# Optimization experiments

Hardware: AMD Instinct MI355X
Metric: run time of the kernel (lower is better)

Reference implementation:

```python
import jax, jax.numpy as jnp
import numpy as np

N = 100000          # nodes
E = 1600000         # edges (before self-loops)
F_IN = 512          # num_node_features
H1, C1 = 8, 8       # layer-1 heads, per-head channels
NUM_CLASSES = 40
NEG_SLOPE = 0.2     # PyG GATConv default


def setup_inputs() -> dict:
    key = jax.random.key(0)
    ks = jax.random.split(key, 10)
    x = jax.random.normal(ks[0], (N, F_IN), jnp.float32)
    edge_index = jax.random.randint(ks[1], (2, E), 0, N, dtype=jnp.int64)
    # Glorot-ish scaled params (matches PyG init scale qualitatively)
    W1 = jax.random.normal(ks[2], (F_IN, H1 * C1), jnp.float32) / np.sqrt(F_IN)
    a_src1 = jax.random.normal(ks[3], (H1, C1), jnp.float32) / np.sqrt(C1)
    a_dst1 = jax.random.normal(ks[4], (H1, C1), jnp.float32) / np.sqrt(C1)
    b1 = jnp.zeros((H1 * C1,), jnp.float32)
    W2 = jax.random.normal(ks[5], (H1 * C1, NUM_CLASSES), jnp.float32) / np.sqrt(H1 * C1)
    a_src2 = jax.random.normal(ks[6], (1, NUM_CLASSES), jnp.float32) / np.sqrt(NUM_CLASSES)
    a_dst2 = jax.random.normal(ks[7], (1, NUM_CLASSES), jnp.float32) / np.sqrt(NUM_CLASSES)
    b2 = jnp.zeros((NUM_CLASSES,), jnp.float32)
    return {"x": x, "edge_index": edge_index, "W1": W1, "a_src1": a_src1,
            "a_dst1": a_dst1, "b1": b1, "W2": W2, "a_src2": a_src2,
            "a_dst2": a_dst2, "b2": b2}


def gat_layer(x, src, dst, W, a_s, a_d, b, concat):
    """PyG GATConv (eval mode: dropout=0). src -> dst messages, softmax over dst."""
    heads, ch = a_s.shape
    n = x.shape[0]
    h = (x @ W).reshape(n, heads, ch)                      # [N,H,C]
    alpha_s = jnp.einsum('nhc,hc->nh', h, a_s)             # [N,H]
    alpha_d = jnp.einsum('nhc,hc->nh', h, a_d)
    e = jax.nn.leaky_relu(alpha_s[src] + alpha_d[dst], NEG_SLOPE)   # [E,H]
    # segment softmax over incoming edges of each dst node
    m = jax.ops.segment_max(e, dst, num_segments=n)        # [N,H]
    p = jnp.exp(e - m[dst])
    s = jax.ops.segment_sum(p, dst, num_segments=n)
    alpha = p / (s[dst] + 1e-16)                           # [E,H]
    out = jax.ops.segment_sum(h[src] * alpha[..., None], dst, num_segments=n)  # [N,H,C]
    out = out.reshape(n, heads * ch) if concat else out.mean(axis=1)
    return out + b


def reference(x, edge_index, W1, a_src1, a_dst1, b1, W2, a_src2, a_dst2, b2):
    n = x.shape[0]
    loops = jnp.arange(n, dtype=edge_index.dtype)
    src = jnp.concatenate([edge_index[0], loops])          # add self-loops (PyG default)
    dst = jnp.concatenate([edge_index[1], loops])
    h = gat_layer(x, src, dst, W1, a_src1, a_dst1, b1, concat=True)
    h = jax.nn.elu(h)
    out = gat_layer(h, src, dst, W2, a_src2, a_dst2, b2, concat=False)
    return jax.nn.log_softmax(out, axis=1)
```

## Files before the change

### kernel.cpp

```cpp
#include <hip/hip_runtime.h>
#include <hip/hip_bf16.h>
#include <hip/hip_fp16.h>

#define F_IN 512
#define HC1 64
#define NH1 8
#define NC 40
#define NEG_SLOPE 0.2f
#define SCAN_CHUNK 2048
#define RADIX_EPB 4096
#define MAXNB 512
#define BCAP 8192

typedef short bf16x8 __attribute__((ext_vector_type(8)));
typedef float f32x4 __attribute__((ext_vector_type(4)));

static __device__ __forceinline__ unsigned short f2b(float f) {
    __hip_bfloat16 h = __float2bfloat16(f);
    return *(unsigned short*)&h;
}
static __device__ __forceinline__ float b2f(unsigned short u) {
    union { unsigned int i; float f; } v;
    v.i = ((unsigned int)u) << 16;
    return v.f;
}
static __device__ __forceinline__ unsigned short f2h(float f) {
    __half h = __float2half(f);
    return *(unsigned short*)&h;
}

__device__ __forceinline__ float lrelu(float e) { return e > 0.f ? e : NEG_SLOPE * e; }

__global__ void prep(const float* __restrict__ W1, const float* __restrict__ W2,
                     const float* __restrict__ a_s2, const float* __restrict__ a_d2,
                     const int* __restrict__ ei,
                     unsigned short* __restrict__ wst, float* __restrict__ ws2,
                     float* __restrict__ wd2, int* __restrict__ flag) {
    if (blockIdx.x == 16) {
        __shared__ int found;
        if (threadIdx.x == 0) found = 0;
        __syncthreads();
        for (int i = threadIdx.x; i < 4096; i += 256) {
            if (ei[2 * i + 1] != 0) atomicOr(&found, 1);
        }
        __syncthreads();
        if (threadIdx.x == 0) *flag = (found == 0) ? 1 : 0;
        return;
    }
    int t = blockIdx.x * 256 + threadIdx.x;
    {
        int p  = t & 7;
        int n  = (t >> 3) & 63;
        int kb = t >> 9;
        int l  = p ^ (n & 7);
        int k0 = kb * 64 + l * 8;
        unsigned short v[8];
#pragma unroll
        for (int j = 0; j < 8; j++) v[j] = f2b(W1[(size_t)(k0 + j) * HC1 + n]);
        *(uint4*)(wst + ((size_t)(kb * 64 + n) * 64 + p * 8)) = *(uint4*)v;
    }
    if (blockIdx.x == 0 && threadIdx.x < HC1) {
        int c = threadIdx.x;
        float s = 0.f, d = 0.f;
#pragma unroll
        for (int j = 0; j < NC; j++) {
            float w = W2[c * NC + j];
            s += w * a_s2[j];
            d += w * a_d2[j];
        }
        ws2[c] = s;
        wd2[c] = d;
    }
}

__global__ __launch_bounds__(256) void scatter1(const int* __restrict__ ei, const int* __restrict__ flag,
                                                int* __restrict__ deg, int* __restrict__ bcnt,
                                                int* __restrict__ bpk, int E, int NB) {
    __shared__ int cnt[MAXNB];
    __shared__ int gb[MAXNB];
    int tid = threadIdx.x;
    for (int i = tid; i < NB; i += 256) cnt[i] = 0;
    __syncthreads();
    int f = *flag;
    int base = blockIdx.x * RADIX_EPB;
    int pk[16], bk[16], rv[16];
#pragma unroll
    for (int i = 0; i < 16; i++) {
        int e = base + i * 256 + tid;
        if (e < E) {
            int s, d;
            if (f) { s = ei[2 * e]; d = ei[2 * (E + e)]; }
            else   { s = ei[e];     d = ei[E + e]; }
            pk[i] = (s << 8) | (d & 255);
            bk[i] = d >> 8;
            rv[i] = atomicAdd(&cnt[bk[i]], 1);
            atomicAdd(&deg[d], 1);
        }
    }
    __syncthreads();
    for (int i = tid; i < NB; i += 256) {
        int c = cnt[i];
        gb[i] = c ? atomicAdd(&bcnt[i], c) : 0;
    }
    __syncthreads();
#pragma unroll
    for (int i = 0; i < 16; i++) {
        int e = base + i * 256 + tid;
        if (e < E) {
            int pos = gb[bk[i]] + rv[i];
            if (pos < BCAP)
                bpk[(size_t)bk[i] * BCAP + pos] = pk[i];
        }
    }
}

__global__ __launch_bounds__(256) void scan1(const int* __restrict__ deg, int* __restrict__ rowptr,
                                             int* __restrict__ bsums, int n) {
    __shared__ int sbuf[256];
    int tid = threadIdx.x;
    int base = blockIdx.x * SCAN_CHUNK + tid * 8;
    int v[8];
#pragma unroll
    for (int j = 0; j < 8; j++) { int idx = base + j; v[j] = (idx < n) ? deg[idx] : 0; }
    int tsum = 0;
#pragma unroll
    for (int j = 0; j < 8; j++) tsum += v[j];
    sbuf[tid] = tsum;
    __syncthreads();
    for (int off = 1; off < 256; off <<= 1) {
        int t = (tid >= off) ? sbuf[tid - off] : 0;
        __syncthreads();
        sbuf[tid] += t;
        __syncthreads();
    }
    int run = sbuf[tid] - tsum;
#pragma unroll
    for (int j = 0; j < 8; j++) {
        run += v[j];
        int idx = base + j;
        if (idx < n) rowptr[1 + idx] = run;
    }
    if (tid == 255) bsums[blockIdx.x] = sbuf[255];
}

__global__ __launch_bounds__(256) void scan23(int* __restrict__ rowptr,
                                              const int* __restrict__ bsums, int n, int nb) {
    __shared__ int soff[64];
    int tid = threadIdx.x;
    if (tid < 64) {
        int lane = tid;
        int v = (lane < nb) ? bsums[lane] : 0;
        int orig = v;
        for (int off = 1; off < 64; off <<= 1) {
            int t = __shfl_up(v, (unsigned)off, 64);
            if (lane >= off) v += t;
        }
        soff[lane] = v - orig;
    }
    __syncthreads();
    int i = blockIdx.x * 256 + tid;
    if (i < n) {
        rowptr[1 + i] += soff[i >> 11];
        if (i == 0) rowptr[0] = 0;
    }
}

__global__ __launch_bounds__(256) void scatter2(const int* __restrict__ bpk,
                                                const int* __restrict__ bcnt,
                                                const int* __restrict__ rowptr,
                                                int* __restrict__ col, int Nn) {
    __shared__ int cur[256];
    int b = blockIdx.x;
    int node0 = b << 8;
    int tid = threadIdx.x;
    int nlast = min(node0 + 256, Nn);
    if (node0 + tid < nlast) cur[tid] = rowptr[node0 + tid];
    __syncthreads();
    int cnt = min(bcnt[b], BCAP);
    const int* bp = bpk + (size_t)b * BCAP;
    for (int j = tid; j < cnt; j += 256) {
        int pk = bp[j];
        int pos = atomicAdd(&cur[pk & 255], 1);
        col[pos] = (int)((unsigned)pk >> 8);
    }
}

__global__ __launch_bounds__(256) void gemm1(const float* __restrict__ x,
                                             const unsigned short* __restrict__ wst,
                                             const float* __restrict__ a_s, const float* __restrict__ a_d,
                                             unsigned short* __restrict__ h1, float* __restrict__ as1,
                                             float* __restrict__ ad1, int Nn) {
    __shared__ __align__(16) unsigned short smem[8192];
    unsigned short* xs = smem;
    unsigned short* ws = smem + 4096;
    int tid = threadIdx.x;
    int m0 = blockIdx.x * 64;
    int w = tid >> 6, lane = tid & 63;
    int quad = lane >> 4, mr = lane & 15;
    f32x4 acc[4];
#pragma unroll
    for (int i = 0; i < 4; i++) acc[i] = (f32x4){0.f, 0.f, 0.f, 0.f};

    int srow = tid >> 2;
    int sseg = tid & 3;
    bool rok = (m0 + srow) < Nn;
    const float* xrow = x + (size_t)(m0 + srow) * F_IN + sseg * 16;
    int swzw = (srow & 7) << 4;
    int swzr = (mr & 7) << 4;

    for (int kb = 0; kb < 8; kb++) {
        float4 xv0, xv1, xv2, xv3;
        if (rok) {
            const float4* xp = (const float4*)(xrow + kb * 64);
            xv0 = xp[0]; xv1 = xp[1]; xv2 = xp[2]; xv3 = xp[3];
        } else {
            xv0 = xv1 = xv2 = xv3 = make_float4(0.f, 0.f, 0.f, 0.f);
        }
        const uint4* wp = (const uint4*)(wst + (size_t)kb * 4096);
        uint4 wv0 = wp[tid];
        uint4 wv1 = wp[tid + 256];
        __syncthreads();
        {
            unsigned short bx[16];
            bx[0]  = f2b(xv0.x); bx[1]  = f2b(xv0.y); bx[2]  = f2b(xv0.z); bx[3]  = f2b(xv0.w);
            bx[4]  = f2b(xv1.x); bx[5]  = f2b(xv1.y); bx[6]  = f2b(xv1.z); bx[7]  = f2b(xv1.w);
            bx[8]  = f2b(xv2.x); bx[9]  = f2b(xv2.y); bx[10] = f2b(xv2.z); bx[11] = f2b(xv2.w);
            bx[12] = f2b(xv3.x); bx[13] = f2b(xv3.y); bx[14] = f2b(xv3.z); bx[15] = f2b(xv3.w);
            unsigned short* xr = xs + srow * 64;
            *(uint4*)(xr + ((((sseg * 32)      ) ^ swzw) >> 1)) = *(uint4*)&bx[0];
            *(uint4*)(xr + ((((sseg * 32) + 16 ) ^ swzw) >> 1)) = *(uint4*)&bx[8];
            ((uint4*)ws)[tid]       = wv0;
            ((uint4*)ws)[tid + 256] = wv1;
        }
        __syncthreads();
#pragma unroll
        for (int ks = 0; ks < 2; ks++) {
            int kc = ks * 64 + quad * 16;
            int co = (kc ^ swzr) >> 1;
            bf16x8 a = *(const bf16x8*)(xs + (w * 16 + mr) * 64 + co);
#pragma unroll
            for (int nb = 0; nb < 4; nb++) {
                bf16x8 b = *(const bf16x8*)(ws + (nb * 16 + mr) * 64 + co);
                acc[nb] = __builtin_amdgcn_mfma_f32_16x16x32_bf16(a, b, acc[nb], 0, 0, 0);
            }
        }
    }
    __syncthreads();
    unsigned short (*hs)[72] = (unsigned short(*)[72])smem;
#pragma unroll
    for (int nb = 0; nb < 4; nb++)
#pragma unroll
        for (int r = 0; r < 4; r++)
            hs[w * 16 + quad * 4 + r][nb * 16 + mr] = f2b(acc[nb][r]);
    __syncthreads();
    {
        if (rok) {
            uint4 v0 = *(const uint4*)&hs[srow][sseg * 16];
            uint4 v1 = *(const uint4*)&hs[srow][sseg * 16 + 8];
            uint4* dst = (uint4*)(h1 + (size_t)(m0 + srow) * HC1 + sseg * 16);
            dst[0] = v0;
            dst[1] = v1;
        }
    }
    for (int i = tid; i < 512; i += 256) {
        int row = i >> 3, hh = i & 7;
        if (m0 + row < Nn) {
            float s = 0.f, d = 0.f;
#pragma unroll
            for (int c = 0; c < 8; c++) {
                float v = b2f(hs[row][hh * 8 + c]);
                s += v * a_s[hh * 8 + c];
                d += v * a_d[hh * 8 + c];
            }
            as1[(size_t)(m0 + row) * NH1 + hh] = s;
            ad1[(size_t)(m0 + row) * NH1 + hh] = d;
        }
    }
}

__global__ __launch_bounds__(256) void agg1(const unsigned short* __restrict__ h1,
                                            const float* __restrict__ as1,
                                            const float* __restrict__ ad1, const int* __restrict__ rowptr,
                                            const int* __restrict__ col, const float* __restrict__ b1,
                                            const float* __restrict__ ws2, const float* __restrict__ wd2,
                                            unsigned short* __restrict__ h2b, float* __restrict__ as2,
                                            float* __restrict__ ad2, int Nn) {
    __shared__ float pbuf[4][NH1 * 68];
    int w = threadIdx.x >> 6;
    int wave = (blockIdx.x * 256 + threadIdx.x) >> 6;
    int lane = threadIdx.x & 63;
    if (wave >= Nn) return;
    int d = wave;
    int jb = rowptr[d], je = rowptr[d + 1];
    int half = lane >> 5;
    int cl = lane & 31;
    int head = cl >> 2;
    const float4* as4 = (const float4*)as1;
    const float4* ad4 = (const float4*)ad1;

    float4 dd0 = ad4[d * 2], dd1 = ad4[d * 2 + 1];
    float adh[8] = {dd0.x, dd0.y, dd0.z, dd0.w, dd1.x, dd1.y, dd1.z, dd1.w};
    float4 sd0 = as4[d * 2], sd1 = as4[d * 2 + 1];
    float svh[8] = {sd0.x, sd0.y, sd0.z, sd0.w, sd1.x, sd1.y, sd1.z, sd1.w};
    float e0[8];
#pragma unroll
    for (int h = 0; h < NH1; h++) e0[h] = lrelu(svh[h] + adh[h]);

    float acc0, acc1, ss;
    {
        unsigned gv = *(const unsigned*)(h1 + (size_t)d * HC1 + 2 * cl);
        union { unsigned i; float f; } lo, hi;
        lo.i = gv << 16; hi.i = gv & 0xffff0000u;
        if (half == 0) { acc0 = lo.f; acc1 = hi.f; ss = 1.f; }
        else           { acc0 = 0.f;  acc1 = 0.f;  ss = 0.f; }
    }
    float* pb = pbuf[w];

    for (int c0 = jb; c0 < je; c0 += 64) {
        int nc = min(64, je - c0);
        int srcv = d;
        if (lane < nc) {
            unsigned u = (unsigned)col[c0 + lane];
            srcv = (u < (unsigned)Nn) ? (int)u : d;
            float4 a0 = as4[srcv * 2], a1 = as4[srcv * 2 + 1];
            float ev[8] = {a0.x, a0.y, a0.z, a0.w, a1.x, a1.y, a1.z, a1.w};
#pragma unroll
            for (int h = 0; h < NH1; h++)
                pb[h * 68 + lane] = __expf(lrelu(ev[h] + adh[h]) - e0[h]);
        } else {
#pragma unroll
            for (int h = 0; h < NH1; h++) pb[h * 68 + lane] = 0.f;
        }
        int ncp = (nc + 15) & ~15;
        for (int jj = 0; jj < ncp; jj += 16) {
            int sarr[8];
            float parr[8];
            unsigned gvv[8];
#pragma unroll
            for (int u4 = 0; u4 < 8; u4++) {
                int idx = jj + 2 * u4 + half;
                sarr[u4] = __shfl(srcv, idx, 64);
                parr[u4] = pb[head * 68 + idx];
            }
#pragma unroll
            for (int u4 = 0; u4 < 8; u4++)
                gvv[u4] = *(const unsigned*)(h1 + (size_t)sarr[u4] * HC1 + 2 * cl);
#pragma unroll
            for (int u4 = 0; u4 < 8; u4++) {
                union { unsigned i; float f; } lo, hi;
                lo.i = gvv[u4] << 16; hi.i = gvv[u4] & 0xffff0000u;
                acc0 += parr[u4] * lo.f;
                acc1 += parr[u4] * hi.f;
                ss += parr[u4];
            }
        }
    }
    acc0 += __shfl_xor(acc0, 32, 64);
    acc1 += __shfl_xor(acc1, 32, 64);
    ss   += __shfl_xor(ss, 32, 64);
    float inv = 1.f / (ss + 1e-16f);
    float o0 = acc0 * inv + b1[2 * cl];
    float o1 = acc1 * inv + b1[2 * cl + 1];
    o0 = o0 > 0.f ? o0 : __expf(o0) - 1.0f;
    o1 = o1 > 0.f ? o1 : __expf(o1) - 1.0f;
    if (half == 0) {
        unsigned pk = (unsigned)f2h(o0) | ((unsigned)f2h(o1) << 16);
        *(unsigned*)(h2b + (size_t)d * HC1 + 2 * cl) = pk;
    }
    float va = o0 * ws2[2 * cl] + o1 * ws2[2 * cl + 1];
    float vd = o0 * wd2[2 * cl] + o1 * wd2[2 * cl + 1];
#pragma unroll
    for (int off = 16; off; off >>= 1) {
        va += __shfl_xor(va, off, 64);
        vd += __shfl_xor(vd, off, 64);
    }
    if (lane == 0) { as2[d] = va; ad2[d] = vd; }
}

__global__ __launch_bounds__(256) void agg2(const unsigned short* __restrict__ h2b,
                                            const float* __restrict__ as2,
                                            const float* __restrict__ ad2, const int* __restrict__ rowptr,
                                            const int* __restrict__ col, const float* __restrict__ W2,
                                            const float* __restrict__ b2,
                                            float* __restrict__ out, int Nn) {
    __shared__ float pbuf[4][64];
    __shared__ float smv[4][64];
    __shared__ float W2s[HC1 * NC];
    int tid = threadIdx.x;
    for (int i = tid; i < HC1 * NC; i += 256) W2s[i] = W2[i];
    __syncthreads();
    int w = tid >> 6;
    int wave = (blockIdx.x * 256 + tid) >> 6;
    int lane = tid & 63;
    if (wave >= Nn) return;
    int d = wave;
    int jb = rowptr[d], je = rowptr[d + 1];
    int half = lane >> 5;
    int cl = lane & 31;
    float adv = ad2[d];
    float e0 = lrelu(as2[d] + adv);
    float acc0, acc1, ss;
    {
        unsigned gv = *(const unsigned*)(h2b + (size_t)d * HC1 + 2 * cl);
        union { unsigned u; __half2 h; } cv; cv.u = gv;
        float2 ff = __half22float2(cv.h);
        if (half == 0) { acc0 = ff.x; acc1 = ff.y; ss = 1.f; }
        else           { acc0 = 0.f;  acc1 = 0.f;  ss = 0.f; }
    }
    float* pb = pbuf[w];

    for (int c0 = jb; c0 < je; c0 += 64) {
        int nc = min(64, je - c0);
        int srcv = d;
        if (lane < nc) {
            unsigned u = (unsigned)col[c0 + lane];
            srcv = (u < (unsigned)Nn) ? (int)u : d;
            pb[lane] = __expf(lrelu(as2[srcv] + adv) - e0);
        } else {
            pb[lane] = 0.f;
        }
        int ncp = (nc + 15) & ~15;
        for (int jj = 0; jj < ncp; jj += 16) {
            int sarr[8];
            float parr[8];
            unsigned gvv[8];
#pragma unroll
            for (int u4 = 0; u4 < 8; u4++) {
                int idx = jj + 2 * u4 + half;
                sarr[u4] = __shfl(srcv, idx, 64);
                parr[u4] = pb[idx];
            }
#pragma unroll
            for (int u4 = 0; u4 < 8; u4++)
                gvv[u4] = *(const unsigned*)(h2b + (size_t)sarr[u4] * HC1 + 2 * cl);
#pragma unroll
            for (int u4 = 0; u4 < 8; u4++) {
                union { unsigned u; __half2 h; } cv; cv.u = gvv[u4];
                float2 ff = __half22float2(cv.h);
                acc0 += parr[u4] * ff.x;
                acc1 += parr[u4] * ff.y;
                ss += parr[u4];
            }
        }
    }
    acc0 += __shfl_xor(acc0, 32, 64);
    acc1 += __shfl_xor(acc1, 32, 64);
    ss   += __shfl_xor(ss, 32, 64);
    float inv = 1.f / (ss + 1e-16f);
    if (half == 0) {
        smv[w][2 * cl]     = acc0 * inv;
        smv[w][2 * cl + 1] = acc1 * inv;
    }
    float o = 0.f;
    if (lane < NC) {
        o = b2[lane];
        const float* sv = smv[w];
#pragma unroll
        for (int c = 0; c < HC1; c++) o += sv[c] * W2s[c * NC + lane];
    }
    float vm = (lane < NC) ? o : -1e30f;
#pragma unroll
    for (int off = 32; off; off >>= 1) vm = fmaxf(vm, __shfl_xor(vm, off, 64));
    float ex = (lane < NC) ? __expf(o - vm) : 0.f;
#pragma unroll
    for (int off = 32; off; off >>= 1) ex += __shfl_xor(ex, off, 64);
    float lsm = o - vm - __logf(ex);
    if (lane < NC) out[(size_t)d * NC + lane] = lsm;
}

extern "C" void kernel_launch(void* const* d_in, const int* in_sizes, int n_in,
                              void* d_out, int out_size, void* d_ws, size_t ws_size,
                              hipStream_t stream) {
    const float* x      = (const float*)d_in[0];
    const int*   ei     = (const int*)d_in[1];
    const float* W1     = (const float*)d_in[2];
    const float* a_src1 = (const float*)d_in[3];
    const float* a_dst1 = (const float*)d_in[4];
    const float* b1     = (const float*)d_in[5];
    const float* W2     = (const float*)d_in[6];
    const float* a_src2 = (const float*)d_in[7];
    const float* a_dst2 = (const float*)d_in[8];
    const float* b2     = (const float*)d_in[9];
    float* out = (float*)d_out;

    const int N = in_sizes[0] / F_IN;
    const int E = in_sizes[1] / 2;
    const int NB = (N + 255) >> 8;

    char* p = (char*)d_ws;
    auto alloc = [&](size_t bytes) -> void* {
        void* r = (void*)p;
        p += (bytes + 255) & ~(size_t)255;
        return r;
    };
    int* deg    = (int*)alloc((size_t)N * 4);
    int* bcnt   = (int*)alloc((size_t)MAXNB * 4);
    int* rowptr = (int*)alloc(((size_t)N + 1) * 4);
    int* bsums  = (int*)alloc(64 * 4);
    int* flag   = (int*)alloc(256);
    int* bpk    = (int*)alloc((size_t)NB * BCAP * 4);
    int* col    = (int*)alloc((size_t)E * 4);
    unsigned short* h1  = (unsigned short*)alloc((size_t)N * HC1 * 2);
    float* as1  = (float*)alloc((size_t)N * NH1 * 4);
    float* ad1  = (float*)alloc((size_t)N * NH1 * 4);
    unsigned short* h2b = (unsigned short*)alloc((size_t)N * HC1 * 2);
    float* as2  = (float*)alloc((size_t)N * 4);
    float* ad2  = (float*)alloc((size_t)N * 4);
    unsigned short* wst = (unsigned short*)alloc(8 * 64 * 64 * 2);
    float* ws2  = (float*)alloc(HC1 * 4);
    float* wd2  = (float*)alloc(HC1 * 4);

    size_t zlen = (size_t)((char*)(bcnt + MAXNB) - (char*)deg);
    hipMemsetAsync(deg, 0, zlen, stream);
    prep<<<17, 256, 0, stream>>>(W1, W2, a_src2, a_dst2, ei, wst, ws2, wd2, flag);
    scatter1<<<(E + RADIX_EPB - 1) / RADIX_EPB, 256, 0, stream>>>(ei, flag, deg, bcnt, bpk, E, NB);
    int nb = (N + SCAN_CHUNK - 1) / SCAN_CHUNK;
    scan1<<<nb, 256, 0, stream>>>(deg, rowptr, bsums, N);
    scan23<<<(N + 255) / 256, 256, 0, stream>>>(rowptr, bsums, N, nb);
    scatter2<<<NB, 256, 0, stream>>>(bpk, bcnt, rowptr, col, N);

    gemm1<<<(N + 63) / 64, 256, 0, stream>>>(x, wst, a_src1, a_dst1, h1, as1, ad1, N);
    agg1<<<(N + 3) / 4, 256, 0, stream>>>(h1, as1, ad1, rowptr, col, b1, ws2, wd2, h2b, as2, ad2, N);

    agg2<<<(N + 3) / 4, 256, 0, stream>>>(h2b, as2, ad2, rowptr, col, W2, b2, out, N);
}
```

Baseline: 581.8 us.

## Split feature channels into four slices and aggregate each slice in its own pass

The hidden features and attention logits move to a slice-major layout: four slices of 16 channels, each 32 bytes per node. Aggregation for both layers runs as four per-slice kernel launches, so each pass gathers from a smaller working set that fits in cache better. Layer 2 writes unnormalised partial sums to a float buffer, and a separate fin kernel applies the normalisation, the W2 projection and log-softmax. In exchange, the edge list and attention exponentials are re-read and recomputed in every pass, there are more launches, and layer-2 logits are accumulated across passes with atomics.

```diff
diff --git a/kernel.cpp b/kernel.cpp
--- a/kernel.cpp
+++ b/kernel.cpp
@@ -27,6 +27,10 @@
 static __device__ __forceinline__ unsigned short f2h(float f) {
     __half h = __float2half(f);
     return *(unsigned short*)&h;
+}
+static __device__ __forceinline__ float h2f(unsigned short u) {
+    __half h = *(__half*)&u;
+    return __half2float(h);
 }
 
 __device__ __forceinline__ float lrelu(float e) { return e > 0.f ? e : NEG_SLOPE * e; }
@@ -188,8 +192,8 @@
 __global__ __launch_bounds__(256) void gemm1(const float* __restrict__ x,
                                              const unsigned short* __restrict__ wst,
                                              const float* __restrict__ a_s, const float* __restrict__ a_d,
-                                             unsigned short* __restrict__ h1, float* __restrict__ as1,
-                                             float* __restrict__ ad1, int Nn) {
+                                             unsigned short* __restrict__ h1s, float* __restrict__ as1s,
+                                             float* __restrict__ ad1s, int Nn) {
     __shared__ __align__(16) unsigned short smem[8192];
     unsigned short* xs = smem;
     unsigned short* ws = smem + 4096;
@@ -257,7 +261,7 @@
         if (rok) {
             uint4 v0 = *(const uint4*)&hs[srow][sseg * 16];
             uint4 v1 = *(const uint4*)&hs[srow][sseg * 16 + 8];
-            uint4* dst = (uint4*)(h1 + (size_t)(m0 + srow) * HC1 + sseg * 16);
+            uint4* dst = (uint4*)(h1s + ((size_t)sseg * Nn + (m0 + srow)) * 16);
             dst[0] = v0;
             dst[1] = v1;
         }
@@ -272,120 +276,140 @@
                 s += v * a_s[hh * 8 + c];
                 d += v * a_d[hh * 8 + c];
             }
-            as1[(size_t)(m0 + row) * NH1 + hh] = s;
-            ad1[(size_t)(m0 + row) * NH1 + hh] = d;
-        }
-    }
-}
-
-__global__ __launch_bounds__(256) void agg1(const unsigned short* __restrict__ h1,
-                                            const float* __restrict__ as1,
-                                            const float* __restrict__ ad1, const int* __restrict__ rowptr,
-                                            const int* __restrict__ col, const float* __restrict__ b1,
-                                            const float* __restrict__ ws2, const float* __restrict__ wd2,
-                                            unsigned short* __restrict__ h2b, float* __restrict__ as2,
-                                            float* __restrict__ ad2, int Nn) {
-    __shared__ float pbuf[4][NH1 * 68];
-    int w = threadIdx.x >> 6;
+            size_t idx = ((size_t)(hh >> 1) * Nn + (m0 + row)) * 2 + (hh & 1);
+            as1s[idx] = s;
+            ad1s[idx] = d;
+        }
+    }
+}
+
+__global__ __launch_bounds__(256) void agg1p(const unsigned short* __restrict__ h1s,
+                                             const float* __restrict__ as1s,
+                                             const float* __restrict__ ad1s,
+                                             const int* __restrict__ rowptr, const int* __restrict__ col,
+                                             const float* __restrict__ b1,
+                                             const float* __restrict__ ws2, const float* __restrict__ wd2,
+                                             unsigned short* __restrict__ h2s, float* __restrict__ as2,
+                                             float* __restrict__ ad2, int Nn, int k) {
     int wave = (blockIdx.x * 256 + threadIdx.x) >> 6;
     int lane = threadIdx.x & 63;
     if (wave >= Nn) return;
     int d = wave;
+    int g = lane >> 3, cl = lane & 7;
+    int hl = cl >> 2;
+    const unsigned short* hsl = h1s + (size_t)k * Nn * 16;
+    const float* asl = as1s + (size_t)k * Nn * 2;
+    const float* adl = ad1s + (size_t)k * Nn * 2;
+    float adv = adl[(size_t)d * 2 + hl];
+    float e0 = lrelu(asl[(size_t)d * 2 + hl] + adv);
     int jb = rowptr[d], je = rowptr[d + 1];
-    int half = lane >> 5;
-    int cl = lane & 31;
-    int head = cl >> 2;
-    const float4* as4 = (const float4*)as1;
-    const float4* ad4 = (const float4*)ad1;
-
-    float4 dd0 = ad4[d * 2], dd1 = ad4[d * 2 + 1];
-    float adh[8] = {dd0.x, dd0.y, dd0.z, dd0.w, dd1.x, dd1.y, dd1.z, dd1.w};
-    float4 sd0 = as4[d * 2], sd1 = as4[d * 2 + 1];
-    float svh[8] = {sd0.x, sd0.y, sd0.z, sd0.w, sd1.x, sd1.y, sd1.z, sd1.w};
-    float e0[8];
-#pragma unroll
-    for (int h = 0; h < NH1; h++) e0[h] = lrelu(svh[h] + adh[h]);
-
-    float acc0, acc1, ss;
-    {
-        unsigned gv = *(const unsigned*)(h1 + (size_t)d * HC1 + 2 * cl);
-        union { unsigned i; float f; } lo, hi;
-        lo.i = gv << 16; hi.i = gv & 0xffff0000u;
-        if (half == 0) { acc0 = lo.f; acc1 = hi.f; ss = 1.f; }
-        else           { acc0 = 0.f;  acc1 = 0.f;  ss = 0.f; }
-    }
-    float* pb = pbuf[w];
-
-    for (int c0 = jb; c0 < je; c0 += 64) {
-        int nc = min(64, je - c0);
-        int srcv = d;
-        if (lane < nc) {
-            unsigned u = (unsigned)col[c0 + lane];
-            srcv = (u < (unsigned)Nn) ? (int)u : d;
-            float4 a0 = as4[srcv * 2], a1 = as4[srcv * 2 + 1];
-            float ev[8] = {a0.x, a0.y, a0.z, a0.w, a1.x, a1.y, a1.z, a1.w};
-#pragma unroll
-            for (int h = 0; h < NH1; h++)
-                pb[h * 68 + lane] = __expf(lrelu(ev[h] + adh[h]) - e0[h]);
-        } else {
-#pragma unroll
-            for (int h = 0; h < NH1; h++) pb[h * 68 + lane] = 0.f;
-        }
-        int ncp = (nc + 15) & ~15;
-        for (int jj = 0; jj < ncp; jj += 16) {
-            int sarr[8];
-            float parr[8];
-            unsigned gvv[8];
-#pragma unroll
-            for (int u4 = 0; u4 < 8; u4++) {
-                int idx = jj + 2 * u4 + half;
-                sarr[u4] = __shfl(srcv, idx, 64);
-                parr[u4] = pb[head * 68 + idx];
-            }
-#pragma unroll
-            for (int u4 = 0; u4 < 8; u4++)
-                gvv[u4] = *(const unsigned*)(h1 + (size_t)sarr[u4] * HC1 + 2 * cl);
-#pragma unroll
-            for (int u4 = 0; u4 < 8; u4++) {
-                union { unsigned i; float f; } lo, hi;
-                lo.i = gvv[u4] << 16; hi.i = gvv[u4] & 0xffff0000u;
-                acc0 += parr[u4] * lo.f;
-                acc1 += parr[u4] * hi.f;
-                ss += parr[u4];
-            }
-        }
-    }
-    acc0 += __shfl_xor(acc0, 32, 64);
-    acc1 += __shfl_xor(acc1, 32, 64);
-    ss   += __shfl_xor(ss, 32, 64);
-    float inv = 1.f / (ss + 1e-16f);
-    float o0 = acc0 * inv + b1[2 * cl];
-    float o1 = acc1 * inv + b1[2 * cl + 1];
-    o0 = o0 > 0.f ? o0 : __expf(o0) - 1.0f;
-    o1 = o1 > 0.f ? o1 : __expf(o1) - 1.0f;
-    if (half == 0) {
+    float acc0 = 0.f, acc1 = 0.f, ss = 0.f;
+    if (g == 0) {
+        unsigned gv = *(const unsigned*)(hsl + (size_t)d * 16 + 2 * cl);
+        acc0 = b2f((unsigned short)(gv & 0xffff));
+        acc1 = b2f((unsigned short)(gv >> 16));
+        ss = 1.f;
+    }
+    for (int c = jb; c < je; c += 16) {
+        int eA = c + g, eB = c + 8 + g;
+        bool vA = eA < je, vB = eB < je;
+        int sA = d, sB = d;
+        if (vA) { unsigned u = (unsigned)col[eA]; sA = (u < (unsigned)Nn) ? (int)u : d; }
+        if (vB) { unsigned u = (unsigned)col[eB]; sB = (u < (unsigned)Nn) ? (int)u : d; }
+        float aA = asl[(size_t)sA * 2 + hl];
+        float aB = asl[(size_t)sB * 2 + hl];
+        unsigned gA = *(const unsigned*)(hsl + (size_t)sA * 16 + 2 * cl);
+        unsigned gB = *(const unsigned*)(hsl + (size_t)sB * 16 + 2 * cl);
+        float pA = vA ? __expf(lrelu(aA + adv) - e0) : 0.f;
+        float pB = vB ? __expf(lrelu(aB + adv) - e0) : 0.f;
+        acc0 += pA * b2f((unsigned short)(gA & 0xffff)) + pB * b2f((unsigned short)(gB & 0xffff));
+        acc1 += pA * b2f((unsigned short)(gA >> 16))   + pB * b2f((unsigned short)(gB >> 16));
+        ss += pA + pB;
+    }
+#pragma unroll
+    for (int off = 8; off <= 32; off <<= 1) {
+        acc0 += __shfl_xor(acc0, off, 64);
+        acc1 += __shfl_xor(acc1, off, 64);
+        ss   += __shfl_xor(ss, off, 64);
+    }
+    if (g == 0) {
+        float inv = 1.f / (ss + 1e-16f);
+        float o0 = acc0 * inv + b1[k * 16 + 2 * cl];
+        float o1 = acc1 * inv + b1[k * 16 + 2 * cl + 1];
+        o0 = o0 > 0.f ? o0 : __expf(o0) - 1.0f;
+        o1 = o1 > 0.f ? o1 : __expf(o1) - 1.0f;
         unsigned pk = (unsigned)f2h(o0) | ((unsigned)f2h(o1) << 16);
-        *(unsigned*)(h2b + (size_t)d * HC1 + 2 * cl) = pk;
-    }
-    float va = o0 * ws2[2 * cl] + o1 * ws2[2 * cl + 1];
-    float vd = o0 * wd2[2 * cl] + o1 * wd2[2 * cl + 1];
-#pragma unroll
-    for (int off = 16; off; off >>= 1) {
-        va += __shfl_xor(va, off, 64);
-        vd += __shfl_xor(vd, off, 64);
-    }
-    if (lane == 0) { as2[d] = va; ad2[d] = vd; }
-}
-
-__global__ __launch_bounds__(256) void agg2(const unsigned short* __restrict__ h2b,
-                                            const float* __restrict__ as2,
-                                            const float* __restrict__ ad2, const int* __restrict__ rowptr,
-                                            const int* __restrict__ col, const float* __restrict__ W2,
-                                            const float* __restrict__ b2,
-                                            float* __restrict__ out, int Nn) {
-    __shared__ float pbuf[4][64];
-    __shared__ float smv[4][64];
+        *(unsigned*)(h2s + ((size_t)k * Nn + d) * 16 + 2 * cl) = pk;
+        float va = o0 * ws2[k * 16 + 2 * cl] + o1 * ws2[k * 16 + 2 * cl + 1];
+        float vd = o0 * wd2[k * 16 + 2 * cl] + o1 * wd2[k * 16 + 2 * cl + 1];
+#pragma unroll
+        for (int off = 1; off <= 4; off <<= 1) {
+            va += __shfl_xor(va, off, 64);
+            vd += __shfl_xor(vd, off, 64);
+        }
+        if (lane == 0) {
+            if (k == 0) { as2[d] = va; ad2[d] = vd; }
+            else        { atomicAdd(&as2[d], va); atomicAdd(&ad2[d], vd); }
+        }
+    }
+}
+
+__global__ __launch_bounds__(256) void agg2p(const unsigned short* __restrict__ h2s,
+                                             const float* __restrict__ as2,
+                                             const float* __restrict__ ad2,
+                                             const int* __restrict__ rowptr, const int* __restrict__ col,
+                                             float* __restrict__ hbar, float* __restrict__ ssum2,
+                                             int Nn, int k) {
+    int wave = (blockIdx.x * 256 + threadIdx.x) >> 6;
+    int lane = threadIdx.x & 63;
+    if (wave >= Nn) return;
+    int d = wave;
+    int g = lane >> 3, cl = lane & 7;
+    const unsigned short* hsl = h2s + (size_t)k * Nn * 16;
+    float adv = ad2[d];
+    float e0 = lrelu(as2[d] + adv);
+    int jb = rowptr[d], je = rowptr[d + 1];
+    float acc0 = 0.f, acc1 = 0.f, ss = 0.f;
+    if (g == 0) {
+        unsigned gv = *(const unsigned*)(hsl + (size_t)d * 16 + 2 * cl);
+        acc0 = h2f((unsigned short)(gv & 0xffff));
+        acc1 = h2f((unsigned short)(gv >> 16));
+        ss = 1.f;
+    }
+    for (int c = jb; c < je; c += 16) {
+        int eA = c + g, eB = c + 8 + g;
+        bool vA = eA < je, vB = eB < je;
+        int sA = d, sB = d;
+        if (vA) { unsigned u = (unsigned)col[eA]; sA = (u < (unsigned)Nn) ? (int)u : d; }
+        if (vB) { unsigned u = (unsigned)col[eB]; sB = (u < (unsigned)Nn) ? (int)u : d; }
+        float aA = as2[sA];
+        float aB = as2[sB];
+        unsigned gA = *(const unsigned*)(hsl + (size_t)sA * 16 + 2 * cl);
+        unsigned gB = *(const unsigned*)(hsl + (size_t)sB * 16 + 2 * cl);
+        float pA = vA ? __expf(lrelu(aA + adv) - e0) : 0.f;
+        float pB = vB ? __expf(lrelu(aB + adv) - e0) : 0.f;
+        acc0 += pA * h2f((unsigned short)(gA & 0xffff)) + pB * h2f((unsigned short)(gB & 0xffff));
+        acc1 += pA * h2f((unsigned short)(gA >> 16))   + pB * h2f((unsigned short)(gB >> 16));
+        ss += pA + pB;
+    }
+#pragma unroll
+    for (int off = 8; off <= 32; off <<= 1) {
+        acc0 += __shfl_xor(acc0, off, 64);
+        acc1 += __shfl_xor(acc1, off, 64);
+        ss   += __shfl_xor(ss, off, 64);
+    }
+    if (g == 0) {
+        *(float2*)(hbar + ((size_t)k * Nn + d) * 16 + 2 * cl) = make_float2(acc0, acc1);
+        if (k == 0 && cl == 0) ssum2[d] = ss;
+    }
+}
+
+__global__ __launch_bounds__(256) void fin(const float* __restrict__ hbar,
+                                           const float* __restrict__ ssum2,
+                                           const float* __restrict__ W2, const float* __restrict__ b2,
+                                           float* __restrict__ out, int Nn) {
     __shared__ float W2s[HC1 * NC];
+    __shared__ float hv[4][HC1];
     int tid = threadIdx.x;
     for (int i = tid; i < HC1 * NC; i += 256) W2s[i] = W2[i];
     __syncthreads();
@@ -394,69 +418,15 @@
     int lane = tid & 63;
     if (wave >= Nn) return;
     int d = wave;
-    int jb = rowptr[d], je = rowptr[d + 1];
-    int half = lane >> 5;
-    int cl = lane & 31;
-    float adv = ad2[d];
-    float e0 = lrelu(as2[d] + adv);
-    float acc0, acc1, ss;
-    {
-        unsigned gv = *(const unsigned*)(h2b + (size_t)d * HC1 + 2 * cl);
-        union { unsigned u; __half2 h; } cv; cv.u = gv;
-        float2 ff = __half22float2(cv.h);
-        if (half == 0) { acc0 = ff.x; acc1 = ff.y; ss = 1.f; }
-        else           { acc0 = 0.f;  acc1 = 0.f;  ss = 0.f; }
-    }
-    float* pb = pbuf[w];
-
-    for (int c0 = jb; c0 < je; c0 += 64) {
-        int nc = min(64, je - c0);
-        int srcv = d;
-        if (lane < nc) {
-            unsigned u = (unsigned)col[c0 + lane];
-            srcv = (u < (unsigned)Nn) ? (int)u : d;
-            pb[lane] = __expf(lrelu(as2[srcv] + adv) - e0);
-        } else {
-            pb[lane] = 0.f;
-        }
-        int ncp = (nc + 15) & ~15;
-        for (int jj = 0; jj < ncp; jj += 16) {
-            int sarr[8];
-            float parr[8];
-            unsigned gvv[8];
-#pragma unroll
-            for (int u4 = 0; u4 < 8; u4++) {
-                int idx = jj + 2 * u4 + half;
-                sarr[u4] = __shfl(srcv, idx, 64);
-                parr[u4] = pb[idx];
-            }
-#pragma unroll
-            for (int u4 = 0; u4 < 8; u4++)
-                gvv[u4] = *(const unsigned*)(h2b + (size_t)sarr[u4] * HC1 + 2 * cl);
-#pragma unroll
-            for (int u4 = 0; u4 < 8; u4++) {
-                union { unsigned u; __half2 h; } cv; cv.u = gvv[u4];
-                float2 ff = __half22float2(cv.h);
-                acc0 += parr[u4] * ff.x;
-                acc1 += parr[u4] * ff.y;
-                ss += parr[u4];
-            }
-        }
-    }
-    acc0 += __shfl_xor(acc0, 32, 64);
-    acc1 += __shfl_xor(acc1, 32, 64);
-    ss   += __shfl_xor(ss, 32, 64);
-    float inv = 1.f / (ss + 1e-16f);
-    if (half == 0) {
-        smv[w][2 * cl]     = acc0 * inv;
-        smv[w][2 * cl + 1] = acc1 * inv;
-    }
+    hv[w][lane] = hbar[((size_t)(lane >> 4) * Nn + d) * 16 + (lane & 15)];
+    float inv = 1.f / (ssum2[d] + 1e-16f);
     float o = 0.f;
     if (lane < NC) {
-        o = b2[lane];
-        const float* sv = smv[w];
-#pragma unroll
-        for (int c = 0; c < HC1; c++) o += sv[c] * W2s[c * NC + lane];
+        float dot = 0.f;
+        const float* sv = hv[w];
+#pragma unroll
+        for (int c = 0; c < HC1; c++) dot += sv[c] * W2s[c * NC + lane];
+        o = b2[lane] + inv * dot;
     }
     float vm = (lane < NC) ? o : -1e30f;
 #pragma unroll
@@ -500,12 +470,14 @@
     int* flag   = (int*)alloc(256);
     int* bpk    = (int*)alloc((size_t)NB * BCAP * 4);
     int* col    = (int*)alloc((size_t)E * 4);
-    unsigned short* h1  = (unsigned short*)alloc((size_t)N * HC1 * 2);
-    float* as1  = (float*)alloc((size_t)N * NH1 * 4);
-    float* ad1  = (float*)alloc((size_t)N * NH1 * 4);
-    unsigned short* h2b = (unsigned short*)alloc((size_t)N * HC1 * 2);
+    unsigned short* h1s = (unsigned short*)alloc((size_t)4 * N * 16 * 2);
+    float* as1s = (float*)alloc((size_t)4 * N * 2 * 4);
+    float* ad1s = (float*)alloc((size_t)4 * N * 2 * 4);
+    unsigned short* h2s = (unsigned short*)alloc((size_t)4 * N * 16 * 2);
     float* as2  = (float*)alloc((size_t)N * 4);
     float* ad2  = (float*)alloc((size_t)N * 4);
+    float* ssum2 = (float*)alloc((size_t)N * 4);
+    float* hbar = (float*)alloc((size_t)4 * N * 16 * 4);
     unsigned short* wst = (unsigned short*)alloc(8 * 64 * 64 * 2);
     float* ws2  = (float*)alloc(HC1 * 4);
     float* wd2  = (float*)alloc(HC1 * 4);
@@ -519,8 +491,13 @@
     scan23<<<(N + 255) / 256, 256, 0, stream>>>(rowptr, bsums, N, nb);
     scatter2<<<NB, 256, 0, stream>>>(bpk, bcnt, rowptr, col, N);
 
-    gemm1<<<(N + 63) / 64, 256, 0, stream>>>(x, wst, a_src1, a_dst1, h1, as1, ad1, N);
-    agg1<<<(N + 3) / 4, 256, 0, stream>>>(h1, as1, ad1, rowptr, col, b1, ws2, wd2, h2b, as2, ad2, N);
-
-    agg2<<<(N + 3) / 4, 256, 0, stream>>>(h2b, as2, ad2, rowptr, col, W2, b2, out, N);
-}
+    gemm1<<<(N + 63) / 64, 256, 0, stream>>>(x, wst, a_src1, a_dst1, h1s, as1s, ad1s, N);
+    int gagg = (N + 3) / 4;
+    for (int k = 0; k < 4; k++)
+        agg1p<<<gagg, 256, 0, stream>>>(h1s, as1s, ad1s, rowptr, col, b1, ws2, wd2,
+                                        h2s, as2, ad2, N, k);
+
+    for (int k = 0; k < 4; k++)
+        agg2p<<<gagg, 256, 0, stream>>>(h2s, as2, ad2, rowptr, col, hbar, ssum2, N, k);
+    fin<<<gagg, 256, 0, stream>>>(hbar, ssum2, W2, b2, out, N);
+}
```

After: 805.2 us. 1.38x slower.
